# Performance work log

Hardware: AMD Instinct MI355X
Metric: run time of the kernel (lower is better)

Reference implementation:

```python
import jax, jax.numpy as jnp
import numpy as np

E = 200000      # n_edges
IN = 128        # input_nf
HID = 32        # hidden_nf
H = 4           # att_heads
OUT = 128       # output_nf
MAXK = 16       # MAX_K neighbor slots


def setup_inputs() -> dict:
    key = jax.random.key(0)
    ks = jax.random.split(key, 12)
    Z = jax.random.normal(ks[0], (E, IN), dtype=jnp.float32)
    idx = jax.random.randint(ks[1], (E, 2, MAXK), 0, E)
    red = jax.random.uniform(ks[2], (E, 1, MAXK)) < 0.15
    klist = jnp.where(red, -1, idx).astype(jnp.int64)
    s = 0.05  # xavier-ish scale
    Wq = jax.random.normal(ks[3], (H, HID, IN), dtype=jnp.float32) * s
    Wk = jax.random.normal(ks[4], (H, HID, IN), dtype=jnp.float32) * s
    Wv = jax.random.normal(ks[5], (H, HID, IN), dtype=jnp.float32) * s
    Wb = jax.random.normal(ks[6], (H, 1, IN), dtype=jnp.float32) * s
    Wg = jax.random.normal(ks[7], (H, HID, IN), dtype=jnp.float32) * s
    bg = jnp.zeros((H, HID), dtype=jnp.float32)
    Wout = jax.random.normal(ks[8], (OUT, H * HID), dtype=jnp.float32) * s
    bout = jnp.zeros((OUT,), dtype=jnp.float32)
    return {"Z": Z, "klist": klist, "Wq": Wq, "Wk": Wk, "Wv": Wv,
            "Wb": Wb, "Wg": Wg, "bg": bg, "Wout": Wout, "bout": bout}


def reference(Z, klist, Wq, Wk, Wv, Wb, Wg, bg, Wout, bout):
    idx_i, idx_j = klist[:, 0], klist[:, 1]          # (E, K)
    red = idx_i == -1
    valid = (~red).astype(Z.dtype)[..., None]        # (E, K, 1)
    ii = jnp.where(red, 0, idx_i)
    jj = jnp.where(red, 0, idx_j)
    scale = 1.0 / np.sqrt(HID)
    outs = []
    for h in range(H):  # att_heads: small fixed loop over structurally distinct heads
        q = Z @ Wq[h].T                              # (E, HID)
        k = Z @ Wk[h].T
        v = Z @ Wv[h].T
        b = (Z @ Wb[h].T)[:, 0]                      # (E,)
        g = jax.nn.sigmoid(Z @ Wg[h].T + bg[h])      # (E, HID)
        tri_k = jnp.take(k, ii, axis=0) * valid      # (E, K, HID), redundant slots zeroed
        tri_v = jnp.take(v, ii, axis=0) * valid
        tri_b = jnp.take(b, jj, axis=0) * valid[..., 0]  # (E, K)
        scores = scale * jnp.einsum('eh,ekh->ek', q, tri_k) + tri_b
        alpha = jax.nn.softmax(scores, axis=1)       # (E, K)
        att = jnp.einsum('ek,ekh->eh', alpha, tri_v) # (E, HID)
        outs.append(g * att)
    out = jnp.concatenate(outs, axis=-1) @ Wout.T + bout  # (E, OUT)
    # dropout is identity in eval mode
    return out
```

## Files before the change

kernel.cpp:

```cpp
#include <hip/hip_runtime.h>
#include <stdint.h>

#define EDGES 200000
#define INF   128
#define HID   32
#define NHEAD 4
#define OUTF  128
#define MAXK  16

#define NPAD  528
#define NTILES 33

typedef unsigned short u16;
typedef __attribute__((ext_vector_type(8))) short bf16x8;
typedef __attribute__((ext_vector_type(4))) float f32x4;

__device__ __forceinline__ u16 f2bf(float f) {
  union { float f; uint32_t u; } v; v.f = f;
  uint32_t u = v.u;
  return (u16)((u + 0x7FFFu + ((u >> 16) & 1u)) >> 16);
}
__device__ __forceinline__ float bf2f(u16 s) {
  union { uint32_t u; float f; } v; v.u = ((uint32_t)s) << 16;
  return v.f;
}
__device__ __forceinline__ float bflo(uint32_t p) {
  union { uint32_t u; float f; } v; v.u = p << 16;
  return v.f;
}
__device__ __forceinline__ float bfhi(uint32_t p) {
  union { uint32_t u; float f; } v; v.u = p & 0xFFFF0000u;
  return v.f;
}

template <int CTRL>
__device__ __forceinline__ float dpp_add(float x) {
  int y = __builtin_amdgcn_update_dpp(0, __builtin_bit_cast(int, x),
                                      CTRL, 0xF, 0xF, true);
  return x + __builtin_bit_cast(float, y);
}
__device__ __forceinline__ float row16_sum(float x) {
  x = dpp_add<0xB1>(x);
  x = dpp_add<0x4E>(x);
  x = dpp_add<0x141>(x);
  x = dpp_add<0x140>(x);
  return x;
}

__global__ __launch_bounds__(256) void prep_kernel(
    const float* __restrict__ Wq, const float* __restrict__ Wk,
    const float* __restrict__ Wv, const float* __restrict__ Wb,
    const float* __restrict__ Wg, const float* __restrict__ Wout,
    u16* __restrict__ Wc, u16* __restrict__ Woutb)
{
  int t = blockIdx.x * 256 + threadIdx.x;
  if (t < NPAD * INF) {
    int n = t >> 7, k = t & 127;
    float v = 0.0f;
    if (n < 128)       v = Wq[n * 128 + k];
    else if (n < 256)  v = Wg[(n - 128) * 128 + k];
    else if (n < 512) {
      int m = n - 256, h = m >> 6, c = m & 63;
      v = (c < 32) ? Wk[(h * 32 + c) * 128 + k] : Wv[(h * 32 + (c - 32)) * 128 + k];
    } else if (n < 516) v = Wb[(n - 512) * 128 + k];
    Wc[t] = f2bf(v);
  } else if (t < NPAD * INF + OUTF * 128) {
    int u = t - NPAD * INF;
    Woutb[u] = f2bf(Wout[u]);
  }
}

__global__ __launch_bounds__(256) void proj_kernel(
    const float* __restrict__ Z, const u16* __restrict__ Wc,
    const float* __restrict__ bg,
    u16* __restrict__ qb, u16* __restrict__ gb,
    u16* __restrict__ kvb, float* __restrict__ bb)
{
  const int wid = threadIdx.x >> 6, lane = threadIdx.x & 63;
  const int ml = lane & 15, blk = lane >> 4;
  const long e0 = (long)blockIdx.x * 128 + wid * 32;

  bf16x8 afr[2][4];
#pragma unroll
  for (int s = 0; s < 2; ++s) {
    long er = e0 + s * 16 + ml; if (er > EDGES - 1) er = EDGES - 1;
    const float* zp = Z + er * INF + blk * 8;
#pragma unroll
    for (int kk = 0; kk < 4; ++kk) {
      float4 f0 = *(const float4*)(zp + kk * 32);
      float4 f1 = *(const float4*)(zp + kk * 32 + 4);
      bf16x8 a;
      a[0] = (short)f2bf(f0.x); a[1] = (short)f2bf(f0.y);
      a[2] = (short)f2bf(f0.z); a[3] = (short)f2bf(f0.w);
      a[4] = (short)f2bf(f1.x); a[5] = (short)f2bf(f1.y);
      a[6] = (short)f2bf(f1.z); a[7] = (short)f2bf(f1.w);
      afr[s][kk] = a;
    }
  }

  for (int nt = 0; nt < NTILES; ++nt) {
    bf16x8 bfr[4];
#pragma unroll
    for (int kk = 0; kk < 4; ++kk)
      bfr[kk] = *(const bf16x8*)(Wc + (nt * 16 + ml) * INF + kk * 32 + blk * 8);

    f32x4 acc[2];
    acc[0] = (f32x4){0.f, 0.f, 0.f, 0.f};
    acc[1] = (f32x4){0.f, 0.f, 0.f, 0.f};
#pragma unroll
    for (int kk = 0; kk < 4; ++kk) {
      acc[0] = __builtin_amdgcn_mfma_f32_16x16x32_bf16(afr[0][kk], bfr[kk], acc[0], 0, 0, 0);
      acc[1] = __builtin_amdgcn_mfma_f32_16x16x32_bf16(afr[1][kk], bfr[kk], acc[1], 0, 0, 0);
    }

    const int n = nt * 16 + ml;
#pragma unroll
    for (int s = 0; s < 2; ++s) {
#pragma unroll
      for (int r = 0; r < 4; ++r) {
        long e = e0 + s * 16 + blk * 4 + r;
        if (e >= EDGES) continue;
        float val = acc[s][r];
        if (n < 128) {
          qb[e * 128 + n] = f2bf(val);
        } else if (n < 256) {
          float sg = 1.0f / (1.0f + __expf(-(val + bg[n - 128])));
          gb[e * 128 + (n - 128)] = f2bf(sg);
        } else if (n < 512) {
          kvb[e * 256 + (n - 256)] = f2bf(val);
        } else if (n < 516) {
          bb[e * 4 + (n - 512)] = val;
        }
      }
    }
  }
}

__global__ __launch_bounds__(256) void attn_kernel(
    const int* __restrict__ klist, const u16* qb,
    const u16* __restrict__ gb, const u16* __restrict__ kvb,
    const float* __restrict__ bb, u16* xb)
{
  const int wid = threadIdx.x >> 6;
  const int lane = threadIdx.x & 63;
  int e = blockIdx.x * 4 + wid;
  e = __builtin_amdgcn_readfirstlane(e);
  if (e >= EDGES) return;

  const int h = lane >> 4;
  const uint32_t q2 = *(const uint32_t*)(qb + (size_t)e * 128 + 2 * lane);
  const uint32_t g2 = *(const uint32_t*)(gb + (size_t)e * 128 + 2 * lane);
  const float q0 = bflo(q2), q1 = bfhi(q2);
  const int kvo = h * 64 + (lane & 15) * 2;
  const float scale = 0.17677669529663687f;

  float sc[MAXK];
  uint32_t vvm[MAXK];
  const int* kl = klist + (size_t)e * 32;
#pragma unroll
  for (int nb = 0; nb < MAXK; ++nb) {
    const int ii = kl[nb];
    const int jj = kl[16 + nb];
    const bool valid = (ii >= 0);
    const int is = valid ? ii : 0;
    const int js = valid ? jj : 0;
    const u16* kvrow = kvb + (size_t)is * 256;
    uint32_t kki = *(const uint32_t*)(kvrow + kvo);
    uint32_t vvi = *(const uint32_t*)(kvrow + kvo + 32);
    float p = q0 * bflo(kki) + q1 * bfhi(kki);
    p = row16_sum(p);
    float bj = bb[(size_t)js * 4 + h];
    sc[nb]  = valid ? (scale * p + bj) : 0.0f;
    vvm[nb] = valid ? vvi : 0u;
  }

  float m = sc[0];
#pragma unroll
  for (int nb = 1; nb < MAXK; ++nb) m = fmaxf(m, sc[nb]);
  float s = 0.f, a0 = 0.f, a1 = 0.f;
#pragma unroll
  for (int nb = 0; nb < MAXK; ++nb) {
    float al = __expf(sc[nb] - m);
    s += al;
    a0 += al * bflo(vvm[nb]);
    a1 += al * bfhi(vvm[nb]);
  }
  float inv = 1.0f / s;
  u16 x0 = f2bf(bflo(g2) * a0 * inv);
  u16 x1 = f2bf(bfhi(g2) * a1 * inv);
  uint32_t xo = (uint32_t)x0 | ((uint32_t)x1 << 16);
  *(uint32_t*)(xb + (size_t)e * 128 + 2 * lane) = xo;
}

__global__ __launch_bounds__(256) void outgemm_kernel(
    const u16* xb, const u16* __restrict__ Woutb,
    const float* __restrict__ bout, float* __restrict__ out)
{
  const int wid = threadIdx.x >> 6, lane = threadIdx.x & 63;
  const int ml = lane & 15, blk = lane >> 4;
  const long e0 = (long)blockIdx.x * 128 + wid * 32;

  bf16x8 afr[2][4];
#pragma unroll
  for (int s = 0; s < 2; ++s) {
    long er = e0 + s * 16 + ml; if (er > EDGES - 1) er = EDGES - 1;
#pragma unroll
    for (int kk = 0; kk < 4; ++kk)
      afr[s][kk] = *(const bf16x8*)(xb + er * 128 + kk * 32 + blk * 8);
  }

#pragma unroll
  for (int nt = 0; nt < 8; ++nt) {
    bf16x8 bfr[4];
#pragma unroll
    for (int kk = 0; kk < 4; ++kk)
      bfr[kk] = *(const bf16x8*)(Woutb + (nt * 16 + ml) * 128 + kk * 32 + blk * 8);

    f32x4 acc[2];
    acc[0] = (f32x4){0.f, 0.f, 0.f, 0.f};
    acc[1] = (f32x4){0.f, 0.f, 0.f, 0.f};
#pragma unroll
    for (int kk = 0; kk < 4; ++kk) {
      acc[0] = __builtin_amdgcn_mfma_f32_16x16x32_bf16(afr[0][kk], bfr[kk], acc[0], 0, 0, 0);
      acc[1] = __builtin_amdgcn_mfma_f32_16x16x32_bf16(afr[1][kk], bfr[kk], acc[1], 0, 0, 0);
    }

    const int o = nt * 16 + ml;
    const float bo = bout[o];
#pragma unroll
    for (int s = 0; s < 2; ++s) {
#pragma unroll
      for (int r = 0; r < 4; ++r) {
        long e = e0 + s * 16 + blk * 4 + r;
        if (e < EDGES) out[e * 128 + o] = acc[s][r] + bo;
      }
    }
  }
}

extern "C" void kernel_launch(void* const* d_in, const int* in_sizes, int n_in,
                              void* d_out, int out_size, void* d_ws, size_t ws_size,
                              hipStream_t stream) {
  const float* Z     = (const float*)d_in[0];
  const int*   klist = (const int*)  d_in[1];
  const float* Wq    = (const float*)d_in[2];
  const float* Wk    = (const float*)d_in[3];
  const float* Wv    = (const float*)d_in[4];
  const float* Wb    = (const float*)d_in[5];
  const float* Wg    = (const float*)d_in[6];
  const float* bg    = (const float*)d_in[7];
  const float* Wout  = (const float*)d_in[8];
  const float* bout  = (const float*)d_in[9];
  float* out = (float*)d_out;

  char* ws = (char*)d_ws;
  u16*   Wc    = (u16*)(ws);
  u16*   Woutb = (u16*)(ws + 135168);
  u16*   qb    = (u16*)(ws + 167936);
  u16*   gb    = (u16*)(ws + 51367936);
  u16*   kvb   = (u16*)(ws + 102567936);
  float* bb    = (float*)(ws + 204967936);
  u16*   xb    = qb;

  prep_kernel<<<(NPAD * INF + OUTF * 128 + 255) / 256, 256, 0, stream>>>(
      Wq, Wk, Wv, Wb, Wg, Wout, Wc, Woutb);
  proj_kernel<<<(EDGES + 127) / 128, 256, 0, stream>>>(
      Z, Wc, bg, qb, gb, kvb, bb);
  attn_kernel<<<(EDGES + 3) / 4, 256, 0, stream>>>(
      klist, qb, gb, kvb, bb, xb);
  outgemm_kernel<<<(EDGES + 127) / 128, 256, 0, stream>>>(
      xb, Woutb, bout, out);
}
```

Before: 628.3 us.

## Swap MFMA operands for row-contiguous vector stores and split proj by output segment

```diff
diff --git a/kernel.cpp b/kernel.cpp
--- a/kernel.cpp
+++ b/kernel.cpp
@@ -1,4 +1,5 @@
 #include <hip/hip_runtime.h>
+#include <hip/hip_bf16.h>
 #include <stdint.h>
 
 #define EDGES 200000
@@ -20,10 +21,6 @@
   uint32_t u = v.u;
   return (u16)((u + 0x7FFFu + ((u >> 16) & 1u)) >> 16);
 }
-__device__ __forceinline__ float bf2f(u16 s) {
-  union { uint32_t u; float f; } v; v.u = ((uint32_t)s) << 16;
-  return v.f;
-}
 __device__ __forceinline__ float bflo(uint32_t p) {
   union { uint32_t u; float f; } v; v.u = p << 16;
   return v.f;
@@ -31,6 +28,25 @@
 __device__ __forceinline__ float bfhi(uint32_t p) {
   union { uint32_t u; float f; } v; v.u = p & 0xFFFF0000u;
   return v.f;
+}
+
+__device__ __forceinline__ uint32_t cvtpk_bf16(float lo, float hi) {
+  float2 t; t.x = lo; t.y = hi;
+  __hip_bfloat162 h = __float22bfloat162_rn(t);
+  uint32_t u;
+  __builtin_memcpy(&u, &h, 4);
+  return u;
+}
+__device__ __forceinline__ bf16x8 pack8(float4 f0, float4 f1) {
+  union { uint32_t u[4]; bf16x8 v; } r;
+  r.u[0] = cvtpk_bf16(f0.x, f0.y);
+  r.u[1] = cvtpk_bf16(f0.z, f0.w);
+  r.u[2] = cvtpk_bf16(f1.x, f1.y);
+  r.u[3] = cvtpk_bf16(f1.z, f1.w);
+  return r.v;
+}
+__device__ __forceinline__ float sigm(float x) {
+  return 1.0f / (1.0f + __expf(-x));
 }
 
 template <int CTRL>
@@ -45,6 +61,25 @@
   x = dpp_add<0x141>(x);
   x = dpp_add<0x140>(x);
   return x;
+}
+
+struct AccPair { f32x4 a, b; };
+__device__ __forceinline__ AccPair tile_mm(const u16* __restrict__ W, int row0,
+                                           int ml, int blk,
+                                           const bf16x8 (&zfr)[2][4], int ldw) {
+  bf16x8 wfr[4];
+#pragma unroll
+  for (int kk = 0; kk < 4; ++kk)
+    wfr[kk] = *(const bf16x8*)(W + (size_t)(row0 + ml) * ldw + kk * 32 + blk * 8);
+  AccPair r;
+  r.a = (f32x4){0.f, 0.f, 0.f, 0.f};
+  r.b = (f32x4){0.f, 0.f, 0.f, 0.f};
+#pragma unroll
+  for (int kk = 0; kk < 4; ++kk) {
+    r.a = __builtin_amdgcn_mfma_f32_16x16x32_bf16(wfr[kk], zfr[0][kk], r.a, 0, 0, 0);
+    r.b = __builtin_amdgcn_mfma_f32_16x16x32_bf16(wfr[kk], zfr[1][kk], r.b, 0, 0, 0);
+  }
+  return r;
 }
 
 __global__ __launch_bounds__(256) void prep_kernel(
@@ -79,59 +114,62 @@
   const int wid = threadIdx.x >> 6, lane = threadIdx.x & 63;
   const int ml = lane & 15, blk = lane >> 4;
   const long e0 = (long)blockIdx.x * 128 + wid * 32;
-
-  bf16x8 afr[2][4];
+  if (e0 >= EDGES) return;
+
+  bf16x8 zfr[2][4];
 #pragma unroll
   for (int s = 0; s < 2; ++s) {
-    long er = e0 + s * 16 + ml; if (er > EDGES - 1) er = EDGES - 1;
-    const float* zp = Z + er * INF + blk * 8;
+    const float* zp = Z + (e0 + s * 16 + ml) * INF + blk * 8;
 #pragma unroll
     for (int kk = 0; kk < 4; ++kk) {
       float4 f0 = *(const float4*)(zp + kk * 32);
       float4 f1 = *(const float4*)(zp + kk * 32 + 4);
-      bf16x8 a;
-      a[0] = (short)f2bf(f0.x); a[1] = (short)f2bf(f0.y);
-      a[2] = (short)f2bf(f0.z); a[3] = (short)f2bf(f0.w);
-      a[4] = (short)f2bf(f1.x); a[5] = (short)f2bf(f1.y);
-      a[6] = (short)f2bf(f1.z); a[7] = (short)f2bf(f1.w);
-      afr[s][kk] = a;
+      zfr[s][kk] = pack8(f0, f1);
     }
   }
 
-  for (int nt = 0; nt < NTILES; ++nt) {
-    bf16x8 bfr[4];
-#pragma unroll
-    for (int kk = 0; kk < 4; ++kk)
-      bfr[kk] = *(const bf16x8*)(Wc + (nt * 16 + ml) * INF + kk * 32 + blk * 8);
-
-    f32x4 acc[2];
-    acc[0] = (f32x4){0.f, 0.f, 0.f, 0.f};
-    acc[1] = (f32x4){0.f, 0.f, 0.f, 0.f};
-#pragma unroll
-    for (int kk = 0; kk < 4; ++kk) {
-      acc[0] = __builtin_amdgcn_mfma_f32_16x16x32_bf16(afr[0][kk], bfr[kk], acc[0], 0, 0, 0);
-      acc[1] = __builtin_amdgcn_mfma_f32_16x16x32_bf16(afr[1][kk], bfr[kk], acc[1], 0, 0, 0);
-    }
-
-    const int n = nt * 16 + ml;
-#pragma unroll
-    for (int s = 0; s < 2; ++s) {
-#pragma unroll
-      for (int r = 0; r < 4; ++r) {
-        long e = e0 + s * 16 + blk * 4 + r;
-        if (e >= EDGES) continue;
-        float val = acc[s][r];
-        if (n < 128) {
-          qb[e * 128 + n] = f2bf(val);
-        } else if (n < 256) {
-          float sg = 1.0f / (1.0f + __expf(-(val + bg[n - 128])));
-          gb[e * 128 + (n - 128)] = f2bf(sg);
-        } else if (n < 512) {
-          kvb[e * 256 + (n - 256)] = f2bf(val);
-        } else if (n < 516) {
-          bb[e * 4 + (n - 512)] = val;
-        }
-      }
+  const long eA = e0 + ml, eB = e0 + 16 + ml;
+
+  for (int nt = 0; nt < 8; ++nt) {
+    AccPair acc = tile_mm(Wc, nt * 16, ml, blk, zfr, INF);
+    const int n0 = nt * 16 + blk * 4;
+    uint2 pa, pb;
+    pa.x = cvtpk_bf16(acc.a[0], acc.a[1]); pa.y = cvtpk_bf16(acc.a[2], acc.a[3]);
+    pb.x = cvtpk_bf16(acc.b[0], acc.b[1]); pb.y = cvtpk_bf16(acc.b[2], acc.b[3]);
+    *(uint2*)(qb + eA * 128 + n0) = pa;
+    *(uint2*)(qb + eB * 128 + n0) = pb;
+  }
+
+  for (int nt = 8; nt < 16; ++nt) {
+    AccPair acc = tile_mm(Wc, nt * 16, ml, blk, zfr, INF);
+    const int ng = (nt - 8) * 16 + blk * 4;
+    float4 b4 = *(const float4*)(bg + ng);
+    float a0 = sigm(acc.a[0] + b4.x), a1 = sigm(acc.a[1] + b4.y);
+    float a2 = sigm(acc.a[2] + b4.z), a3 = sigm(acc.a[3] + b4.w);
+    float c0 = sigm(acc.b[0] + b4.x), c1 = sigm(acc.b[1] + b4.y);
+    float c2 = sigm(acc.b[2] + b4.z), c3 = sigm(acc.b[3] + b4.w);
+    uint2 pa, pb;
+    pa.x = cvtpk_bf16(a0, a1); pa.y = cvtpk_bf16(a2, a3);
+    pb.x = cvtpk_bf16(c0, c1); pb.y = cvtpk_bf16(c2, c3);
+    *(uint2*)(gb + eA * 128 + ng) = pa;
+    *(uint2*)(gb + eB * 128 + ng) = pb;
+  }
+
+  for (int nt = 16; nt < 32; ++nt) {
+    AccPair acc = tile_mm(Wc, nt * 16, ml, blk, zfr, INF);
+    const int nk = (nt - 16) * 16 + blk * 4;
+    uint2 pa, pb;
+    pa.x = cvtpk_bf16(acc.a[0], acc.a[1]); pa.y = cvtpk_bf16(acc.a[2], acc.a[3]);
+    pb.x = cvtpk_bf16(acc.b[0], acc.b[1]); pb.y = cvtpk_bf16(acc.b[2], acc.b[3]);
+    *(uint2*)(kvb + eA * 256 + nk) = pa;
+    *(uint2*)(kvb + eB * 256 + nk) = pb;
+  }
+
+  {
+    AccPair acc = tile_mm(Wc, 512, ml, blk, zfr, INF);
+    if (blk == 0) {
+      *(float4*)(bb + eA * 4) = make_float4(acc.a[0], acc.a[1], acc.a[2], acc.a[3]);
+      *(float4*)(bb + eB * 4) = make_float4(acc.b[0], acc.b[1], acc.b[2], acc.b[3]);
     }
   }
 }
@@ -199,42 +237,30 @@
   const int wid = threadIdx.x >> 6, lane = threadIdx.x & 63;
   const int ml = lane & 15, blk = lane >> 4;
   const long e0 = (long)blockIdx.x * 128 + wid * 32;
-
-  bf16x8 afr[2][4];
+  if (e0 >= EDGES) return;
+
+  bf16x8 xfr[2][4];
 #pragma unroll
   for (int s = 0; s < 2; ++s) {
-    long er = e0 + s * 16 + ml; if (er > EDGES - 1) er = EDGES - 1;
+    const u16* xp = xb + (e0 + s * 16 + ml) * 128 + blk * 8;
 #pragma unroll
     for (int kk = 0; kk < 4; ++kk)
-      afr[s][kk] = *(const bf16x8*)(xb + er * 128 + kk * 32 + blk * 8);
-  }
+      xfr[s][kk] = *(const bf16x8*)(xp + kk * 32);
+  }
+
+  const long eA = e0 + ml, eB = e0 + 16 + ml;
 
 #pragma unroll
   for (int nt = 0; nt < 8; ++nt) {
-    bf16x8 bfr[4];
-#pragma unroll
-    for (int kk = 0; kk < 4; ++kk)
-      bfr[kk] = *(const bf16x8*)(Woutb + (nt * 16 + ml) * 128 + kk * 32 + blk * 8);
-
-    f32x4 acc[2];
-    acc[0] = (f32x4){0.f, 0.f, 0.f, 0.f};
-    acc[1] = (f32x4){0.f, 0.f, 0.f, 0.f};
-#pragma unroll
-    for (int kk = 0; kk < 4; ++kk) {
-      acc[0] = __builtin_amdgcn_mfma_f32_16x16x32_bf16(afr[0][kk], bfr[kk], acc[0], 0, 0, 0);
-      acc[1] = __builtin_amdgcn_mfma_f32_16x16x32_bf16(afr[1][kk], bfr[kk], acc[1], 0, 0, 0);
-    }
-
-    const int o = nt * 16 + ml;
-    const float bo = bout[o];
-#pragma unroll
-    for (int s = 0; s < 2; ++s) {
-#pragma unroll
-      for (int r = 0; r < 4; ++r) {
-        long e = e0 + s * 16 + blk * 4 + r;
-        if (e < EDGES) out[e * 128 + o] = acc[s][r] + bo;
-      }
-    }
+    AccPair acc = tile_mm(Woutb, nt * 16, ml, blk, xfr, 128);
+    const int o0 = nt * 16 + blk * 4;
+    float4 b4 = *(const float4*)(bout + o0);
+    float4 ra = make_float4(acc.a[0] + b4.x, acc.a[1] + b4.y,
+                            acc.a[2] + b4.z, acc.a[3] + b4.w);
+    float4 rb = make_float4(acc.b[0] + b4.x, acc.b[1] + b4.y,
+                            acc.b[2] + b4.z, acc.b[3] + b4.w);
+    *(float4*)(out + eA * 128 + o0) = ra;
+    *(float4*)(out + eB * 128 + o0) = rb;
   }
 }
 
```

New measurement: 611.9 us. 1.03x faster.
